# Kernel optimization log

Measured on AMD Instinct MI355X. Metric: run time of the kernel, lower is better.

## Reference

```python
import jax, jax.numpy as jnp
import numpy as np

B, N, C, K = 2, 8192, 128, 16
EPS = 1e-5


def setup_inputs() -> dict:
    key = jax.random.key(0)
    ks = jax.random.split(key, 24)
    s = 1.0 / np.sqrt(C)
    nrm = lambda k, shape, sc: jax.random.normal(k, shape, dtype=jnp.float32) * sc
    return {
        "xyz": jax.random.normal(ks[0], (B, N, 3), dtype=jnp.float32),
        "feat": jax.random.normal(ks[1], (B, N, C), dtype=jnp.float32),
        "Wq": nrm(ks[2], (C, C), s),
        "Wk": nrm(ks[3], (C, C), s),
        "Wv": nrm(ks[4], (C, C), s),
        "pW1": nrm(ks[5], (C, 3), 0.5),
        "pb1": nrm(ks[6], (C,), 0.1),
        "pg": jnp.ones((C,), jnp.float32),
        "pbeta": jnp.zeros((C,), jnp.float32),
        "pmean": nrm(ks[7], (C,), 0.1),
        "pvar": jax.random.uniform(ks[8], (C,), jnp.float32, 0.5, 1.5),
        "pW2": nrm(ks[9], (C, C), s),
        "pb2": nrm(ks[10], (C,), 0.1),
        "aW1": nrm(ks[11], (C, C), s),
        "ab1": nrm(ks[12], (C,), 0.1),
        "ag": jnp.ones((C,), jnp.float32),
        "abeta": jnp.zeros((C,), jnp.float32),
        "amean": nrm(ks[13], (C,), 0.1),
        "avar": jax.random.uniform(ks[14], (C,), jnp.float32, 0.5, 1.5),
        "aW2": nrm(ks[15], (C, C), s),
        "ab2": nrm(ks[16], (C,), 0.1),
        "Wout": nrm(ks[17], (C, C), s),
    }


def _bn(x, g, b, mean, var):
    # eval-mode BatchNorm1d with running stats
    return (x - mean) * jax.lax.rsqrt(var + EPS) * g + b


def _lin(x, W):
    # torch nn.Linear convention: W is [out, in]
    return jnp.einsum('...i,oi->...o', x, W)


def reference(xyz, feat, Wq, Wk, Wv, pW1, pb1, pg, pbeta, pmean, pvar, pW2, pb2,
              aW1, ab1, ag, abeta, amean, avar, aW2, ab2, Wout):
    # KNN via squared distances (||a||^2 + ||b||^2 - 2 a.b), [B,N,N]
    sq = jnp.sum(xyz * xyz, axis=-1)
    dist = sq[:, :, None] + sq[:, None, :] - 2.0 * jnp.einsum('bnd,bmd->bnm', xyz, xyz)
    _, idx = jax.lax.top_k(-dist, K)  # [B,N,K] nearest neighbors

    gather = jax.vmap(lambda pts, i: pts[i])  # [B,N,C],[B,N,K] -> [B,N,K,C]
    nb_xyz = gather(xyz, idx)    # [B,N,K,3]
    nb_feat = gather(feat, idx)  # [B,N,K,C]

    q = _lin(feat, Wq)[:, :, None, :]  # [B,N,1,C]
    k = _lin(nb_feat, Wk)              # [B,N,K,C]
    v = _lin(nb_feat, Wv)              # [B,N,K,C]

    rel = nb_xyz - xyz[:, :, None, :]  # [B,N,K,3]
    pos = _lin(jax.nn.relu(_bn(_lin(rel, pW1) + pb1, pg, pbeta, pmean, pvar)), pW2) + pb2

    attn = q - k + pos
    attn = _lin(jax.nn.relu(_bn(_lin(attn, aW1) + ab1, ag, abeta, amean, avar)), aW2) + ab2
    attn = jax.nn.softmax(attn, axis=2)  # per-channel softmax over K neighbors

    out = jnp.sum(attn * (v + pos), axis=2)  # [B,N,C]
    return _lin(out, Wout)
```

## Files before the change

kernel.cpp:

```cpp
#include <hip/hip_runtime.h>
#include <cstdint>
#include <cstddef>

#define BB 2
#define NN 8192
#define CC 128
#define KK 16
#define EPSV 1e-5f
#define GRP 16
#define GPTS 512
#define GCAP 32

typedef unsigned long long u64;
typedef unsigned int u32;
typedef unsigned short ushort_t;
typedef short short8v __attribute__((ext_vector_type(8)));
typedef float f32x4 __attribute__((ext_vector_type(4)));

__device__ __forceinline__ float med3f(float x, float y, float z) {
  float r;
  asm("v_med3_f32 %0, %1, %2, %3" : "=v"(r) : "v"(x), "v"(y), "v"(z));
  return r;
}

__global__ __launch_bounds__(256) void k_prep(const float* __restrict__ xyz,
                                              float4* __restrict__ xyzw) {
  int t = blockIdx.x * 256 + threadIdx.x;
  if (t >= BB * NN) return;
  float x = xyz[t * 3 + 0], y = xyz[t * 3 + 1], z = xyz[t * 3 + 2];
  float sq = __fadd_rn(__fadd_rn(__fmul_rn(x, x), __fmul_rn(y, y)), __fmul_rn(z, z));
  xyzw[t] = make_float4(x, y, z, sq);
}

__device__ __forceinline__ float distf(const float4& q, const float4& c) {
  float dot = __fadd_rn(__fadd_rn(__fmul_rn(q.x, c.x), __fmul_rn(q.y, c.y)),
                        __fmul_rn(q.z, c.z));
  float d = __fsub_rn(__fadd_rn(q.w, c.w), __fmul_rn(2.0f, dot));
  return fmaxf(d, 0.0f);
}

__device__ __forceinline__ float distq(const float4& p, const float4& c) {
  return fmaf(p.z, c.z, fmaf(p.y, c.y, fmaf(p.x, c.x, p.w + c.w)));
}

__global__ __launch_bounds__(256) void k_thr(const float4* __restrict__ xyzw,
                                             float* __restrict__ thr) {
  __shared__ float part[16][16][16];
  const int tid = threadIdx.x;
  const int qloc = tid & 15;
  const int s = tid >> 4;
  const int n = blockIdx.x * 16 + qloc;
  const int b = n >> 13;
  const float4 q = xyzw[n];
  const float4 p = make_float4(-2.f * q.x, -2.f * q.y, -2.f * q.z, q.w);
  const float4* base = xyzw + b * NN;
  float a[KK];
#pragma unroll
  for (int i = 0; i < KK; ++i) a[i] = 3.4e38f;
  const int j0 = s * 64;
#pragma unroll 4
  for (int i = 0; i < 64; ++i) {
    const float4 c = base[(j0 + i) * 8];
    const float d = distq(p, c);
#pragma unroll
    for (int k = KK - 1; k >= 1; --k) a[k] = med3f(d, a[k - 1], a[k]);
    a[0] = fminf(d, a[0]);
  }
#pragma unroll
  for (int i = 0; i < KK; ++i) part[qloc][s][i] = a[i];
  __syncthreads();
  if (s < 4) {
#pragma unroll
    for (int ss = 1; ss < 4; ++ss)
#pragma unroll
      for (int i = 0; i < KK; ++i) {
        const float d = part[qloc][s + ss * 4][i];
#pragma unroll
        for (int k = KK - 1; k >= 1; --k) a[k] = med3f(d, a[k - 1], a[k]);
        a[0] = fminf(d, a[0]);
      }
#pragma unroll
    for (int i = 0; i < KK; ++i) part[qloc][s][i] = a[i];
  }
  __syncthreads();
  if (s == 0) {
#pragma unroll
    for (int ss = 1; ss < 4; ++ss)
#pragma unroll
      for (int i = 0; i < KK; ++i) {
        const float d = part[qloc][ss][i];
#pragma unroll
        for (int k = KK - 1; k >= 1; --k) a[k] = med3f(d, a[k - 1], a[k]);
        a[0] = fminf(d, a[0]);
      }
    const float t = a[KK - 1];
    thr[n] = t + (5e-4f + 4e-5f * fabsf(t));
  }
}

__global__ __launch_bounds__(256) void k_collect(const float4* __restrict__ xyzw,
                                                 const float* __restrict__ thr,
                                                 u32* __restrict__ cnt8,
                                                 u32* __restrict__ list) {
  __shared__ float4 pts[GPTS];
  const int tid = threadIdx.x;
  const int n = blockIdx.x * 256 + tid;
  const int b = n >> 13;
  const int g = blockIdx.y;
  const int m0 = g * GPTS;
#pragma unroll
  for (int i = 0; i < GPTS / 256; ++i)
    pts[i * 256 + tid] = xyzw[b * NN + m0 + i * 256 + tid];
  const float4 q = xyzw[n];
  const float4 p = make_float4(-2.f * q.x, -2.f * q.y, -2.f * q.z, q.w);
  const float tn = thr[n];
  __syncthreads();
  u32* seg = list + ((size_t)n * GRP + g) * GCAP;
  int cnt = 0;
#pragma unroll 4
  for (int mi = 0; mi < GPTS; ++mi) {
    const float d = distq(p, pts[mi]);
    if (d <= tn) {
      if (cnt < GCAP) seg[cnt] = (u32)(m0 + mi);
      ++cnt;
    }
  }
  cnt8[n * GRP + g] = (u32)cnt;
}

__global__ __launch_bounds__(256) void k_fin(const float4* __restrict__ xyzw,
                                             const u32* __restrict__ cnt8,
                                             const u32* __restrict__ list,
                                             int* __restrict__ idx) {
  __shared__ double part[16][16][16];
  const int tid = threadIdx.x;
  const int qloc = tid & 15;
  const int s = tid >> 4;
  const int n = blockIdx.x * 16 + qloc;
  const int b = n >> 13;
  const float4 q = xyzw[n];
  const int cn = (int)cnt8[n * GRP + s];
  const int cl = (cn < GCAP) ? cn : GCAP;
  const u32* L = list + ((size_t)n * GRP + s) * GCAP;
  double keys[KK];
#pragma unroll
  for (int i = 0; i < KK; ++i) keys[i] = __longlong_as_double(0x7FEFFFFFFFFFFFFFLL);
  for (int j = 0; j < cl; ++j) {
    const u32 m = L[j];
    const float d = distf(q, xyzw[b * NN + m]);
    u64 kb_ = ((u64)__float_as_uint(d) << 32) | m;
    double kd = __longlong_as_double((long long)kb_);
    if (kd < keys[KK - 1]) {
#pragma unroll
      for (int i = 0; i < KK; ++i) {
        double lo = fmin(keys[i], kd);
        kd = fmax(keys[i], kd);
        keys[i] = lo;
      }
    }
  }
#pragma unroll
  for (int i = 0; i < KK; ++i) part[qloc][s][i] = keys[i];
  __syncthreads();
  if (s < 4) {
#pragma unroll
    for (int ss = 1; ss < 4; ++ss)
#pragma unroll
      for (int i = 0; i < KK; ++i) {
        double kd = part[qloc][s + ss * 4][i];
        if (kd < keys[KK - 1]) {
#pragma unroll
          for (int k = 0; k < KK; ++k) {
            double lo = fmin(keys[k], kd);
            kd = fmax(keys[k], kd);
            keys[k] = lo;
          }
        }
      }
#pragma unroll
    for (int i = 0; i < KK; ++i) part[qloc][s][i] = keys[i];
  }
  __syncthreads();
  if (s == 0) {
#pragma unroll
    for (int ss = 1; ss < 4; ++ss)
#pragma unroll
      for (int i = 0; i < KK; ++i) {
        double kd = part[qloc][ss][i];
        if (kd < keys[KK - 1]) {
#pragma unroll
          for (int k = 0; k < KK; ++k) {
            double lo = fmin(keys[k], kd);
            kd = fmax(keys[k], kd);
            keys[k] = lo;
          }
        }
      }
    bool ovf = false;
#pragma unroll
    for (int gg = 0; gg < GRP; ++gg) ovf |= (cnt8[n * GRP + gg] > GCAP);
    if (ovf) {
#pragma unroll
      for (int i = 0; i < KK; ++i) keys[i] = __longlong_as_double(0x7FEFFFFFFFFFFFFFLL);
      for (int mi = 0; mi < NN; ++mi) {
        const float d = distf(q, xyzw[b * NN + mi]);
        u64 kb_ = ((u64)__float_as_uint(d) << 32) | (u32)mi;
        double kd = __longlong_as_double((long long)kb_);
        if (kd < keys[KK - 1]) {
#pragma unroll
          for (int k = 0; k < KK; ++k) {
            double lo = fmin(keys[k], kd);
            kd = fmax(keys[k], kd);
            keys[k] = lo;
          }
        }
      }
    }
#pragma unroll
    for (int j = 0; j < KK; ++j)
      idx[n * KK + j] = (int)((u64)__double_as_longlong(keys[j]) & 0xffffffffu);
  }
}

__global__ __launch_bounds__(128) void k_fold(const float* __restrict__ aW1,
                                              const float* __restrict__ Wq,
                                              const float* __restrict__ Wk,
                                              const float* __restrict__ pW2,
                                              const float* __restrict__ pb2,
                                              float* __restrict__ WqA,
                                              float* __restrict__ WkA,
                                              float* __restrict__ WpA,
                                              float* __restrict__ tvec) {
  const int bx = blockIdx.x;
  const int j = threadIdx.x;
  if (bx == 48) {
    float s = 0.f;
    for (int i = 0; i < 128; ++i) s = fmaf(aW1[j * 128 + i], pb2[i], s);
    tvec[j] = s;
    return;
  }
  const int mat = bx >> 4;
  const int c0 = (bx & 15) * 8;
  const float* S = (mat == 0) ? Wq : (mat == 1) ? Wk : pW2;
  float* D = (mat == 0) ? WqA : (mat == 1) ? WkA : WpA;
  float acc[8];
#pragma unroll
  for (int r = 0; r < 8; ++r) acc[r] = 0.f;
  for (int i = 0; i < 128; ++i) {
    float sv = S[i * 128 + j];
#pragma unroll
    for (int r = 0; r < 8; ++r) acc[r] = fmaf(aW1[(c0 + r) * 128 + i], sv, acc[r]);
  }
#pragma unroll
  for (int r = 0; r < 8; ++r) D[(c0 + r) * 128 + j] = acc[r];
}

__device__ __forceinline__ void splitf(float a, ushort_t& h, ushort_t& l) {
  u32 ab = __float_as_uint(a);
  h = (ushort_t)(ab >> 16);
  float hif = __uint_as_float(ab & 0xffff0000u);
  l = (ushort_t)(__float_as_uint(a - hif) >> 16);
}

__global__ __launch_bounds__(256) void k_packw(
    const float* __restrict__ S0, const float* __restrict__ S1,
    const float* __restrict__ S2, const float* __restrict__ S3,
    const float* __restrict__ S4, const float* __restrict__ S5,
    const float* __restrict__ S6, ushort_t* __restrict__ Phall,
    ushort_t* __restrict__ Plall) {
  const int bx = blockIdx.x;
  const int mat = bx >> 3;
  const int T = bx & 7;
  const float* S;
  switch (mat) {
    case 0: S = S0; break;
    case 1: S = S1; break;
    case 2: S = S2; break;
    case 3: S = S3; break;
    case 4: S = S4; break;
    case 5: S = S5; break;
    default: S = S6; break;
  }
  const int tid = threadIdx.x;
  const int s = tid >> 4;
  const int lr = tid & 15;
  const int c = T * 16 + lr;
  short8v vh, vl;
#pragma unroll
  for (int e = 0; e < 8; ++e) {
    ushort_t hh, ll;
    splitf(S[c * 128 + s * 8 + e], hh, ll);
    vh[e] = (short)hh;
    vl[e] = (short)ll;
  }
  const int po = mat * 16384 + T * 2048 + s * 128 + lr * 8;
  *(short8v*)&Phall[po] = vh;
  *(short8v*)&Plall[po] = vl;
}

template <int ITERS>
__device__ __forceinline__ void stage_rows(const float4* __restrict__ G4,
                                           ushort_t* Bh, ushort_t* Bl, int tid) {
#pragma unroll
  for (int i = 0; i < ITERS; ++i) {
    int f = i * 256 + tid;
    int r = f >> 5, k4 = f & 31;
    float4 v = G4[f];
    ushort_t h0, l0, h1, l1, h2, l2, h3, l3;
    splitf(v.x, h0, l0);
    splitf(v.y, h1, l1);
    splitf(v.z, h2, l2);
    splitf(v.w, h3, l3);
    int slot = k4 >> 1;
    int sub = (k4 & 1) * 4;
    int base = r * 128 + ((slot ^ (r & 15)) * 8) + sub;
    *(uint2*)&Bh[base] = make_uint2((u32)h0 | ((u32)h1 << 16), (u32)h2 | ((u32)h3 << 16));
    *(uint2*)&Bl[base] = make_uint2((u32)l0 | ((u32)l1 << 16), (u32)l2 | ((u32)l3 << 16));
  }
}

__device__ __forceinline__ void gemm64g(const ushort_t* ABh, const ushort_t* ABl,
                                        const ushort_t* __restrict__ Ph,
                                        const ushort_t* __restrict__ Pl,
                                        f32x4 acc[2][4], int tid) {
  const int l = tid & 63, wid = tid >> 6;
  const int wrow = wid >> 1, wcol = wid & 1;
  const int lq = l >> 4, lr = l & 15;
#pragma unroll
  for (int ks = 0; ks < 4; ++ks) {
    const int sw8 = (((ks * 4 + lq) ^ lr) * 8);
    short8v ah[2], al[2], wh[4], wl[4];
#pragma unroll
    for (int ct = 0; ct < 4; ++ct) {
      int off = (wcol * 4 + ct) * 2048 + (ks * 4 + lq) * 128 + lr * 8;
      wh[ct] = *(const short8v*)&Ph[off];
      wl[ct] = *(const short8v*)&Pl[off];
    }
#pragma unroll
    for (int rt = 0; rt < 2; ++rt) {
      int row = wrow * 32 + rt * 16 + lr;
      ah[rt] = *(const short8v*)&ABh[row * 128 + sw8];
      al[rt] = *(const short8v*)&ABl[row * 128 + sw8];
    }
    __builtin_amdgcn_s_setprio(1);
#pragma unroll
    for (int rt = 0; rt < 2; ++rt)
#pragma unroll
      for (int ct = 0; ct < 4; ++ct) {
        acc[rt][ct] = __builtin_amdgcn_mfma_f32_16x16x32_bf16(ah[rt], wh[ct], acc[rt][ct], 0, 0, 0);
        acc[rt][ct] = __builtin_amdgcn_mfma_f32_16x16x32_bf16(ah[rt], wl[ct], acc[rt][ct], 0, 0, 0);
        acc[rt][ct] = __builtin_amdgcn_mfma_f32_16x16x32_bf16(al[rt], wh[ct], acc[rt][ct], 0, 0, 0);
      }
    __builtin_amdgcn_s_setprio(0);
  }
}

template <int NW>
__global__ __launch_bounds__(256) void k_mms(const float* __restrict__ A,
                                             const ushort_t* __restrict__ Phall,
                                             const ushort_t* __restrict__ Plall,
                                             int m0, float* __restrict__ C0,
                                             float* __restrict__ C1,
                                             float* __restrict__ C2) {
  __shared__ ushort_t ABh[16 * 128], ABl[16 * 128];
  const int tid = threadIdx.x;
  const int Rbase = blockIdx.x * 16;
  stage_rows<2>((const float4*)(A + (size_t)Rbase * 128), ABh, ABl, tid);
  __syncthreads();
  const int l = tid & 63, wid = tid >> 6;
  const int lq = l >> 4, lr = l & 15;
  float* Cs[3] = {C0, C1, C2};
#pragma unroll
  for (int w = 0; w < NW; ++w) {
    const ushort_t* Ph = Phall + (size_t)(m0 + w) * 16384;
    const ushort_t* Pl = Plall + (size_t)(m0 + w) * 16384;
    f32x4 acc[2];
#pragma unroll
    for (int ct = 0; ct < 2; ++ct) acc[ct] = (f32x4)0.f;
#pragma unroll
    for (int ks = 0; ks < 4; ++ks) {
      const int sw8 = (((ks * 4 + lq) ^ lr) * 8);
      short8v ah, al, wh[2], wl[2];
#pragma unroll
      for (int ct = 0; ct < 2; ++ct) {
        int off = (wid * 2 + ct) * 2048 + (ks * 4 + lq) * 128 + lr * 8;
        wh[ct] = *(const short8v*)&Ph[off];
        wl[ct] = *(const short8v*)&Pl[off];
      }
      ah = *(const short8v*)&ABh[lr * 128 + sw8];
      al = *(const short8v*)&ABl[lr * 128 + sw8];
#pragma unroll
      for (int ct = 0; ct < 2; ++ct) {
        acc[ct] = __builtin_amdgcn_mfma_f32_16x16x32_bf16(ah, wh[ct], acc[ct], 0, 0, 0);
        acc[ct] = __builtin_amdgcn_mfma_f32_16x16x32_bf16(ah, wl[ct], acc[ct], 0, 0, 0);
        acc[ct] = __builtin_amdgcn_mfma_f32_16x16x32_bf16(al, wh[ct], acc[ct], 0, 0, 0);
      }
    }
#pragma unroll
    for (int ct = 0; ct < 2; ++ct) {
      int c = (wid * 2 + ct) * 16 + lr;
#pragma unroll
      for (int reg = 0; reg < 4; ++reg) {
        int R = Rbase + lq * 4 + reg;
        Cs[w][(size_t)R * 128 + c] = acc[ct][reg];
      }
    }
  }
}

__global__ __launch_bounds__(256, 3) void k_fused(
    const float4* __restrict__ xyzw, const int* __restrict__ idx,
    const float* __restrict__ qbA, const float* __restrict__ kbA,
    const float* __restrict__ vb, const float* __restrict__ pW1,
    const float* __restrict__ pb1, const float* __restrict__ pg,
    const float* __restrict__ pbeta, const float* __restrict__ pm,
    const float* __restrict__ pv, const float* __restrict__ pb2,
    const float* __restrict__ ab1, const float* __restrict__ ag,
    const float* __restrict__ abeta, const float* __restrict__ am,
    const float* __restrict__ av, const float* __restrict__ ab2,
    const float* __restrict__ tvec, const ushort_t* __restrict__ Phall,
    const ushort_t* __restrict__ Plall, float* __restrict__ out) {
  __shared__ ushort_t ABh[64 * 128], ABl[64 * 128];
  __shared__ float4 fW1[128];
  __shared__ float sA[128], tA[128], pB2[128], aB2[128];
  __shared__ int idxs[64];
  const int tid = threadIdx.x;
  const int Qbase = blockIdx.x * 4;
  const int b = Qbase >> 13;

  if (tid < 64) idxs[tid] = idx[Qbase * KK + tid];
  if (tid < 128) {
    int c = tid;
    float s1 = pg[c] / sqrtf(pv[c] + EPSV);
    fW1[c] = make_float4(pW1[c * 3] * s1, pW1[c * 3 + 1] * s1, pW1[c * 3 + 2] * s1,
                         (pb1[c] - pm[c]) * s1 + pbeta[c]);
    float s2 = ag[c] / sqrtf(av[c] + EPSV);
    sA[c] = s2;
    tA[c] = fmaf(s2, ab1[c] + tvec[c] - am[c], abeta[c]);
    pB2[c] = pb2[c];
    aB2[c] = ab2[c];
  }
  __syncthreads();

  {
    int r = tid >> 2, qq = tid & 3;
    int Q = Qbase + (r >> 4);
    int m = idxs[r];
    float4 pq = xyzw[Q];
    float4 pn = xyzw[b * NN + m];
    float rx = pn.x - pq.x, ry = pn.y - pq.y, rz = pn.z - pq.z;
#pragma unroll
    for (int g = 0; g < 4; ++g) {
      short8v vh, vl;
      int c0 = qq * 32 + g * 8;
#pragma unroll
      for (int e = 0; e < 8; ++e) {
        float4 w = fW1[c0 + e];
        float h = fmaxf(fmaf(rz, w.z, fmaf(ry, w.y, fmaf(rx, w.x, w.w))), 0.f);
        ushort_t hh, ll;
        splitf(h, hh, ll);
        vh[e] = (short)hh;
        vl[e] = (short)ll;
      }
      int sw = (c0 >> 3) ^ (r & 15);
      *(short8v*)&ABh[r * 128 + sw * 8] = vh;
      *(short8v*)&ABl[r * 128 + sw * 8] = vl;
    }
  }
  __syncthreads();

  const int l = tid & 63, wid = tid >> 6;
  const int wrow = wid >> 1, wcol = wid & 1;
  const int lq = l >> 4, lr = l & 15;

  f32x4 pos_[2][4], pa_[2][4];
#pragma unroll
  for (int rt = 0; rt < 2; ++rt)
#pragma unroll
    for (int ct = 0; ct < 4; ++ct) {
      pos_[rt][ct] = (f32x4)0.f;
      pa_[rt][ct] = (f32x4)0.f;
    }
  gemm64g(ABh, ABl, Phall, Plall, pos_, tid);
  gemm64g(ABh, ABl, Phall + 16384, Plall + 16384, pa_, tid);
  __syncthreads();

#pragma unroll
  for (int rt = 0; rt < 2; ++rt) {
    int qi_loc = wrow * 2 + rt;
    int Q = Qbase + qi_loc;
    int mr[4];
#pragma unroll
    for (int reg = 0; reg < 4; ++reg) mr[reg] = b * NN + idxs[qi_loc * 16 + lq * 4 + reg];
#pragma unroll
    for (int ct = 0; ct < 4; ++ct) {
      int c = wcol * 64 + ct * 16 + lr;
      float qv = qbA[(size_t)Q * 128 + c];
      float sc = sA[c], tc = tA[c];
#pragma unroll
      for (int reg = 0; reg < 4; ++reg) {
        float u = qv - kbA[(size_t)mr[reg] * 128 + c] + pa_[rt][ct][reg];
        float z = fmaxf(fmaf(u, sc, tc), 0.f);
        ushort_t hh, ll;
        splitf(z, hh, ll);
        int R15 = lq * 4 + reg;
        int row = wrow * 32 + rt * 16 + R15;
        int base = row * 128 + (((c >> 3) ^ R15) * 8) + (c & 7);
        ABh[base] = hh;
        ABl[base] = ll;
      }
    }
  }
  __syncthreads();

  f32x4 acc[2][4];
#pragma unroll
  for (int rt = 0; rt < 2; ++rt)
#pragma unroll
    for (int ct = 0; ct < 4; ++ct) acc[rt][ct] = (f32x4)0.f;
  gemm64g(ABh, ABl, Phall + 32768, Plall + 32768, acc, tid);

  float oo[2][4];
#pragma unroll
  for (int rt = 0; rt < 2; ++rt) {
    int qi_loc = wrow * 2 + rt;
    int mr[4];
#pragma unroll
    for (int reg = 0; reg < 4; ++reg) mr[reg] = b * NN + idxs[qi_loc * 16 + lq * 4 + reg];
#pragma unroll
    for (int ct = 0; ct < 4; ++ct) {
      int c = wcol * 64 + ct * 16 + lr;
      float ab2v = aB2[c];
      float lg[4];
#pragma unroll
      for (int reg = 0; reg < 4; ++reg) lg[reg] = acc[rt][ct][reg] + ab2v;
      float mx = fmaxf(fmaxf(lg[0], lg[1]), fmaxf(lg[2], lg[3]));
      mx = fmaxf(mx, __shfl_xor(mx, 16));
      mx = fmaxf(mx, __shfl_xor(mx, 32));
      float s = 0.f, o = 0.f;
      float pb2v = pB2[c];
#pragma unroll
      for (int reg = 0; reg < 4; ++reg) {
        float e_ = __expf(lg[reg] - mx);
        s += e_;
        float vv = vb[(size_t)mr[reg] * 128 + c] + pos_[rt][ct][reg] + pb2v;
        o = fmaf(e_, vv, o);
      }
      s += __shfl_xor(s, 16);
      s += __shfl_xor(s, 32);
      o += __shfl_xor(o, 16);
      o += __shfl_xor(o, 32);
      oo[rt][ct] = o / s;
    }
  }

  __syncthreads();
  if (lq == 0) {
#pragma unroll
    for (int rt = 0; rt < 2; ++rt) {
      int row = wrow * 2 + rt;
#pragma unroll
      for (int ct = 0; ct < 4; ++ct) {
        int c = wcol * 64 + ct * 16 + lr;
        ushort_t hh, ll;
        splitf(oo[rt][ct], hh, ll);
        int base = row * 128 + (((c >> 3) ^ row) * 8) + (c & 7);
        ABh[base] = hh;
        ABl[base] = ll;
      }
    }
  }
  __syncthreads();

  const ushort_t* Ph6 = Phall + 6 * 16384;
  const ushort_t* Pl6 = Plall + 6 * 16384;
  f32x4 fo[2];
  fo[0] = (f32x4)0.f;
  fo[1] = (f32x4)0.f;
#pragma unroll
  for (int ks = 0; ks < 4; ++ks) {
    const int sw8 = (((ks * 4 + lq) ^ lr) * 8);
    short8v ah = *(const short8v*)&ABh[lr * 128 + sw8];
    short8v al = *(const short8v*)&ABl[lr * 128 + sw8];
#pragma unroll
    for (int ct = 0; ct < 2; ++ct) {
      int off2 = (wid * 2 + ct) * 2048 + (ks * 4 + lq) * 128 + lr * 8;
      short8v wh = *(const short8v*)&Ph6[off2];
      short8v wl = *(const short8v*)&Pl6[off2];
      fo[ct] = __builtin_amdgcn_mfma_f32_16x16x32_bf16(ah, wh, fo[ct], 0, 0, 0);
      fo[ct] = __builtin_amdgcn_mfma_f32_16x16x32_bf16(ah, wl, fo[ct], 0, 0, 0);
      fo[ct] = __builtin_amdgcn_mfma_f32_16x16x32_bf16(al, wh, fo[ct], 0, 0, 0);
    }
  }
  if (lq == 0) {
#pragma unroll
    for (int ct = 0; ct < 2; ++ct) {
      int c = (wid * 2 + ct) * 16 + lr;
#pragma unroll
      for (int reg = 0; reg < 4; ++reg)
        out[(size_t)(Qbase + reg) * 128 + c] = fo[ct][reg];
    }
  }
}

extern "C" void kernel_launch(void* const* d_in, const int* in_sizes, int n_in,
                              void* d_out, int out_size, void* d_ws, size_t ws_size,
                              hipStream_t stream) {
  const float* xyz = (const float*)d_in[0];
  const float* feat = (const float*)d_in[1];
  const float* Wq = (const float*)d_in[2];
  const float* Wk = (const float*)d_in[3];
  const float* Wv = (const float*)d_in[4];
  const float* pW1 = (const float*)d_in[5];
  const float* pb1 = (const float*)d_in[6];
  const float* pg = (const float*)d_in[7];
  const float* pbeta = (const float*)d_in[8];
  const float* pmean = (const float*)d_in[9];
  const float* pvar = (const float*)d_in[10];
  const float* pW2 = (const float*)d_in[11];
  const float* pb2 = (const float*)d_in[12];
  const float* aW1 = (const float*)d_in[13];
  const float* ab1 = (const float*)d_in[14];
  const float* ag = (const float*)d_in[15];
  const float* abeta = (const float*)d_in[16];
  const float* amean = (const float*)d_in[17];
  const float* avar = (const float*)d_in[18];
  const float* aW2 = (const float*)d_in[19];
  const float* ab2 = (const float*)d_in[20];
  const float* Wout = (const float*)d_in[21];
  float* out = (float*)d_out;
  char* ws = (char*)d_ws;

  size_t off = 0;
  auto alloc = [&](size_t bytes) {
    size_t r = off;
    off += (bytes + 255) & ~(size_t)255;
    return r;
  };
  float4* xyzw = (float4*)(ws + alloc((size_t)BB * NN * 16));
  int* idx = (int*)(ws + alloc((size_t)BB * NN * KK * 4));
  size_t o_qb = alloc((size_t)BB * NN * CC * 4);
  size_t o_kb = alloc((size_t)BB * NN * CC * 4);
  size_t o_vb = alloc((size_t)BB * NN * CC * 4);
  size_t o_ob = alloc((size_t)BB * NN * CC * 4);
  float* qbA = (float*)(ws + o_qb);
  float* kbA = (float*)(ws + o_kb);
  float* vb = (float*)(ws + o_vb);
  (void)o_ob;
  u32* list = (u32*)(ws + o_qb);
  float* WqA = (float*)(ws + alloc(128 * 128 * 4));
  float* WkA = (float*)(ws + alloc(128 * 128 * 4));
  float* WpA = (float*)(ws + alloc(128 * 128 * 4));
  float* tvec = (float*)(ws + alloc(128 * 4));
  ushort_t* Phall = (ushort_t*)(ws + alloc(7 * 16384 * 2));
  ushort_t* Plall = (ushort_t*)(ws + alloc(7 * 16384 * 2));
  float* thrbuf = (float*)(ws + alloc((size_t)BB * NN * 4));
  u32* cnt8 = (u32*)(ws + alloc((size_t)BB * NN * GRP * 4));

  k_prep<<<(BB * NN) / 256, 256, 0, stream>>>(xyz, xyzw);
  k_fold<<<49, 128, 0, stream>>>(aW1, Wq, Wk, pW2, pb2, WqA, WkA, WpA, tvec);
  k_packw<<<56, 256, 0, stream>>>(pW2, WpA, aW2, WqA, WkA, Wv, Wout, Phall, Plall);

  k_thr<<<(BB * NN) / 16, 256, 0, stream>>>(xyzw, thrbuf);
  k_collect<<<dim3((BB * NN) / 256, GRP), 256, 0, stream>>>(xyzw, thrbuf, cnt8, list);
  k_fin<<<(BB * NN) / 16, 256, 0, stream>>>(xyzw, cnt8, list, idx);

  k_mms<3><<<(BB * NN) / 16, 256, 0, stream>>>(feat, Phall, Plall, 3, qbA, kbA, vb);

  k_fused<<<(BB * NN * KK) / 64, 256, 0, stream>>>(
      xyzw, idx, qbA, kbA, vb, pW1, pb1, pg, pbeta, pmean, pvar, pb2, ab1, ag,
      abeta, amean, avar, ab2, tvec, Phall, Plall, out);
}
```

Before: 243.1 us.

## Split fused attention kernel across 8 waves with 16 rows per wave

```diff
diff --git a/kernel.cpp b/kernel.cpp
--- a/kernel.cpp
+++ b/kernel.cpp
@@ -319,38 +319,35 @@
   }
 }
 
-__device__ __forceinline__ void gemm64g(const ushort_t* ABh, const ushort_t* ABl,
-                                        const ushort_t* __restrict__ Ph,
-                                        const ushort_t* __restrict__ Pl,
-                                        f32x4 acc[2][4], int tid) {
+__device__ __forceinline__ void gemm64g8(const ushort_t* ABh, const ushort_t* ABl,
+                                         const ushort_t* __restrict__ Ph,
+                                         const ushort_t* __restrict__ Pl,
+                                         f32x4 acc[4], int tid) {
   const int l = tid & 63, wid = tid >> 6;
   const int wrow = wid >> 1, wcol = wid & 1;
   const int lq = l >> 4, lr = l & 15;
 #pragma unroll
   for (int ks = 0; ks < 4; ++ks) {
     const int sw8 = (((ks * 4 + lq) ^ lr) * 8);
-    short8v ah[2], al[2], wh[4], wl[4];
+    short8v ah, al, wh[4], wl[4];
 #pragma unroll
     for (int ct = 0; ct < 4; ++ct) {
       int off = (wcol * 4 + ct) * 2048 + (ks * 4 + lq) * 128 + lr * 8;
       wh[ct] = *(const short8v*)&Ph[off];
       wl[ct] = *(const short8v*)&Pl[off];
     }
-#pragma unroll
-    for (int rt = 0; rt < 2; ++rt) {
-      int row = wrow * 32 + rt * 16 + lr;
-      ah[rt] = *(const short8v*)&ABh[row * 128 + sw8];
-      al[rt] = *(const short8v*)&ABl[row * 128 + sw8];
+    {
+      int row = wrow * 16 + lr;
+      ah = *(const short8v*)&ABh[row * 128 + sw8];
+      al = *(const short8v*)&ABl[row * 128 + sw8];
     }
     __builtin_amdgcn_s_setprio(1);
 #pragma unroll
-    for (int rt = 0; rt < 2; ++rt)
-#pragma unroll
-      for (int ct = 0; ct < 4; ++ct) {
-        acc[rt][ct] = __builtin_amdgcn_mfma_f32_16x16x32_bf16(ah[rt], wh[ct], acc[rt][ct], 0, 0, 0);
-        acc[rt][ct] = __builtin_amdgcn_mfma_f32_16x16x32_bf16(ah[rt], wl[ct], acc[rt][ct], 0, 0, 0);
-        acc[rt][ct] = __builtin_amdgcn_mfma_f32_16x16x32_bf16(al[rt], wh[ct], acc[rt][ct], 0, 0, 0);
-      }
+    for (int ct = 0; ct < 4; ++ct) {
+      acc[ct] = __builtin_amdgcn_mfma_f32_16x16x32_bf16(ah, wh[ct], acc[ct], 0, 0, 0);
+      acc[ct] = __builtin_amdgcn_mfma_f32_16x16x32_bf16(ah, wl[ct], acc[ct], 0, 0, 0);
+      acc[ct] = __builtin_amdgcn_mfma_f32_16x16x32_bf16(al, wh[ct], acc[ct], 0, 0, 0);
+    }
     __builtin_amdgcn_s_setprio(0);
   }
 }
@@ -408,7 +405,7 @@
   }
 }
 
-__global__ __launch_bounds__(256, 3) void k_fused(
+__global__ __launch_bounds__(512, 4) void k_fused(
     const float4* __restrict__ xyzw, const int* __restrict__ idx,
     const float* __restrict__ qbA, const float* __restrict__ kbA,
     const float* __restrict__ vb, const float* __restrict__ pW1,
@@ -443,16 +440,16 @@
   __syncthreads();
 
   {
-    int r = tid >> 2, qq = tid & 3;
+    int r = tid >> 3, qq = tid & 7;
     int Q = Qbase + (r >> 4);
     int m = idxs[r];
     float4 pq = xyzw[Q];
     float4 pn = xyzw[b * NN + m];
     float rx = pn.x - pq.x, ry = pn.y - pq.y, rz = pn.z - pq.z;
 #pragma unroll
-    for (int g = 0; g < 4; ++g) {
+    for (int g = 0; g < 2; ++g) {
       short8v vh, vl;
-      int c0 = qq * 32 + g * 8;
+      int c0 = qq * 16 + g * 8;
 #pragma unroll
       for (int e = 0; e < 8; ++e) {
         float4 w = fW1[c0 + e];
@@ -473,25 +470,21 @@
   const int wrow = wid >> 1, wcol = wid & 1;
   const int lq = l >> 4, lr = l & 15;
 
-  f32x4 pos_[2][4], pa_[2][4];
-#pragma unroll
-  for (int rt = 0; rt < 2; ++rt)
-#pragma unroll
-    for (int ct = 0; ct < 4; ++ct) {
-      pos_[rt][ct] = (f32x4)0.f;
-      pa_[rt][ct] = (f32x4)0.f;
-    }
-  gemm64g(ABh, ABl, Phall, Plall, pos_, tid);
-  gemm64g(ABh, ABl, Phall + 16384, Plall + 16384, pa_, tid);
-  __syncthreads();
-
-#pragma unroll
-  for (int rt = 0; rt < 2; ++rt) {
-    int qi_loc = wrow * 2 + rt;
-    int Q = Qbase + qi_loc;
+  f32x4 pos_[4], pa_[4];
+#pragma unroll
+  for (int ct = 0; ct < 4; ++ct) {
+    pos_[ct] = (f32x4)0.f;
+    pa_[ct] = (f32x4)0.f;
+  }
+  gemm64g8(ABh, ABl, Phall, Plall, pos_, tid);
+  gemm64g8(ABh, ABl, Phall + 16384, Plall + 16384, pa_, tid);
+  __syncthreads();
+
+  {
+    const int Q = Qbase + wrow;
     int mr[4];
 #pragma unroll
-    for (int reg = 0; reg < 4; ++reg) mr[reg] = b * NN + idxs[qi_loc * 16 + lq * 4 + reg];
+    for (int reg = 0; reg < 4; ++reg) mr[reg] = b * NN + idxs[wrow * 16 + lq * 4 + reg];
 #pragma unroll
     for (int ct = 0; ct < 4; ++ct) {
       int c = wcol * 64 + ct * 16 + lr;
@@ -499,12 +492,12 @@
       float sc = sA[c], tc = tA[c];
 #pragma unroll
       for (int reg = 0; reg < 4; ++reg) {
-        float u = qv - kbA[(size_t)mr[reg] * 128 + c] + pa_[rt][ct][reg];
+        float u = qv - kbA[(size_t)mr[reg] * 128 + c] + pa_[ct][reg];
         float z = fmaxf(fmaf(u, sc, tc), 0.f);
         ushort_t hh, ll;
         splitf(z, hh, ll);
         int R15 = lq * 4 + reg;
-        int row = wrow * 32 + rt * 16 + R15;
+        int row = wrow * 16 + R15;
         int base = row * 128 + (((c >> 3) ^ R15) * 8) + (c & 7);
         ABh[base] = hh;
         ABl[base] = ll;
@@ -513,27 +506,23 @@
   }
   __syncthreads();
 
-  f32x4 acc[2][4];
-#pragma unroll
-  for (int rt = 0; rt < 2; ++rt)
-#pragma unroll
-    for (int ct = 0; ct < 4; ++ct) acc[rt][ct] = (f32x4)0.f;
-  gemm64g(ABh, ABl, Phall + 32768, Plall + 32768, acc, tid);
-
-  float oo[2][4];
-#pragma unroll
-  for (int rt = 0; rt < 2; ++rt) {
-    int qi_loc = wrow * 2 + rt;
+  f32x4 acc[4];
+#pragma unroll
+  for (int ct = 0; ct < 4; ++ct) acc[ct] = (f32x4)0.f;
+  gemm64g8(ABh, ABl, Phall + 32768, Plall + 32768, acc, tid);
+
+  float oo[4];
+  {
     int mr[4];
 #pragma unroll
-    for (int reg = 0; reg < 4; ++reg) mr[reg] = b * NN + idxs[qi_loc * 16 + lq * 4 + reg];
+    for (int reg = 0; reg < 4; ++reg) mr[reg] = b * NN + idxs[wrow * 16 + lq * 4 + reg];
 #pragma unroll
     for (int ct = 0; ct < 4; ++ct) {
       int c = wcol * 64 + ct * 16 + lr;
       float ab2v = aB2[c];
       float lg[4];
 #pragma unroll
-      for (int reg = 0; reg < 4; ++reg) lg[reg] = acc[rt][ct][reg] + ab2v;
+      for (int reg = 0; reg < 4; ++reg) lg[reg] = acc[ct][reg] + ab2v;
       float mx = fmaxf(fmaxf(lg[0], lg[1]), fmaxf(lg[2], lg[3]));
       mx = fmaxf(mx, __shfl_xor(mx, 16));
       mx = fmaxf(mx, __shfl_xor(mx, 32));
@@ -543,63 +532,52 @@
       for (int reg = 0; reg < 4; ++reg) {
         float e_ = __expf(lg[reg] - mx);
         s += e_;
-        float vv = vb[(size_t)mr[reg] * 128 + c] + pos_[rt][ct][reg] + pb2v;
+        float vv = vb[(size_t)mr[reg] * 128 + c] + pos_[ct][reg] + pb2v;
         o = fmaf(e_, vv, o);
       }
       s += __shfl_xor(s, 16);
       s += __shfl_xor(s, 32);
       o += __shfl_xor(o, 16);
       o += __shfl_xor(o, 32);
-      oo[rt][ct] = o / s;
+      oo[ct] = o / s;
     }
   }
 
   __syncthreads();
   if (lq == 0) {
-#pragma unroll
-    for (int rt = 0; rt < 2; ++rt) {
-      int row = wrow * 2 + rt;
-#pragma unroll
-      for (int ct = 0; ct < 4; ++ct) {
-        int c = wcol * 64 + ct * 16 + lr;
-        ushort_t hh, ll;
-        splitf(oo[rt][ct], hh, ll);
-        int base = row * 128 + (((c >> 3) ^ row) * 8) + (c & 7);
-        ABh[base] = hh;
-        ABl[base] = ll;
-      }
+    int row = wrow;
+#pragma unroll
+    for (int ct = 0; ct < 4; ++ct) {
+      int c = wcol * 64 + ct * 16 + lr;
+      ushort_t hh, ll;
+      splitf(oo[ct], hh, ll);
+      int base = row * 128 + (((c >> 3) ^ row) * 8) + (c & 7);
+      ABh[base] = hh;
+      ABl[base] = ll;
     }
   }
   __syncthreads();
 
   const ushort_t* Ph6 = Phall + 6 * 16384;
   const ushort_t* Pl6 = Plall + 6 * 16384;
-  f32x4 fo[2];
-  fo[0] = (f32x4)0.f;
-  fo[1] = (f32x4)0.f;
+  f32x4 fo = (f32x4)0.f;
 #pragma unroll
   for (int ks = 0; ks < 4; ++ks) {
     const int sw8 = (((ks * 4 + lq) ^ lr) * 8);
     short8v ah = *(const short8v*)&ABh[lr * 128 + sw8];
     short8v al = *(const short8v*)&ABl[lr * 128 + sw8];
-#pragma unroll
-    for (int ct = 0; ct < 2; ++ct) {
-      int off2 = (wid * 2 + ct) * 2048 + (ks * 4 + lq) * 128 + lr * 8;
-      short8v wh = *(const short8v*)&Ph6[off2];
-      short8v wl = *(const short8v*)&Pl6[off2];
-      fo[ct] = __builtin_amdgcn_mfma_f32_16x16x32_bf16(ah, wh, fo[ct], 0, 0, 0);
-      fo[ct] = __builtin_amdgcn_mfma_f32_16x16x32_bf16(ah, wl, fo[ct], 0, 0, 0);
-      fo[ct] = __builtin_amdgcn_mfma_f32_16x16x32_bf16(al, wh, fo[ct], 0, 0, 0);
-    }
+    int off2 = wid * 2048 + (ks * 4 + lq) * 128 + lr * 8;
+    short8v wh = *(const short8v*)&Ph6[off2];
+    short8v wl = *(const short8v*)&Pl6[off2];
+    fo = __builtin_amdgcn_mfma_f32_16x16x32_bf16(ah, wh, fo, 0, 0, 0);
+    fo = __builtin_amdgcn_mfma_f32_16x16x32_bf16(ah, wl, fo, 0, 0, 0);
+    fo = __builtin_amdgcn_mfma_f32_16x16x32_bf16(al, wh, fo, 0, 0, 0);
   }
   if (lq == 0) {
-#pragma unroll
-    for (int ct = 0; ct < 2; ++ct) {
-      int c = (wid * 2 + ct) * 16 + lr;
-#pragma unroll
-      for (int reg = 0; reg < 4; ++reg)
-        out[(size_t)(Qbase + reg) * 128 + c] = fo[ct][reg];
-    }
+    int c = wid * 16 + lr;
+#pragma unroll
+    for (int reg = 0; reg < 4; ++reg)
+      out[(size_t)(Qbase + reg) * 128 + c] = fo[reg];
   }
 }
 
@@ -667,7 +645,7 @@
 
   k_mms<3><<<(BB * NN) / 16, 256, 0, stream>>>(feat, Phall, Plall, 3, qbA, kbA, vb);
 
-  k_fused<<<(BB * NN * KK) / 64, 256, 0, stream>>>(
+  k_fused<<<(BB * NN * KK) / 64, 512, 0, stream>>>(
       xyzw, idx, qbA, kbA, vb, pW1, pb1, pg, pbeta, pmean, pvar, pb2, ab1, ag,
       abeta, amean, avar, ab2, tvec, Phall, Plall, out);
 }
```

Measured after the change: 296.2 us. 1.22x slower.
